# Optimization experiments

Hardware: AMD Instinct MI355X
Metric: run time of the kernel (lower is better)

The kernel has to match this reference:

```python
import jax, jax.numpy as jnp
import numpy as np

N = 200000
NNZ = 6400000
E = 500000
IN_P, IN_F, IN_N = 62, 37, 37
HID, LAT, DEC_HID = 256, 128, 64


def _p(key, shape, scale=0.05):
    return scale * jax.random.normal(key, shape, dtype=jnp.float32)


def setup_inputs() -> dict:
    key = jax.random.key(0)
    ks = jax.random.split(key, 32)
    inp = {
        'x_process': jax.random.normal(ks[0], (N, IN_P), dtype=jnp.float32),
        'x_file': jax.random.normal(ks[1], (N, IN_F), dtype=jnp.float32),
        'x_network': jax.random.normal(ks[2], (N, IN_N), dtype=jnp.float32),
        'adj_rows': jax.random.randint(ks[3], (NNZ,), 0, N, dtype=jnp.int32),
        'adj_cols': jax.random.randint(ks[4], (NNZ,), 0, N, dtype=jnp.int32),
        'adj_vals': jax.random.uniform(ks[5], (NNZ,), dtype=jnp.float32) / 32.0,
        'edge_src': jax.random.randint(ks[6], (E,), 0, N, dtype=jnp.int32),
        'edge_dst': jax.random.randint(ks[7], (E,), 0, N, dtype=jnp.int32),
        # per-view encoder params (weights stored [in, out])
        'Wp1': _p(ks[8], (IN_P, HID)), 'bp1': jnp.zeros((HID,), jnp.float32),
        'Wp2': _p(ks[9], (HID, LAT)), 'bp2': jnp.zeros((LAT,), jnp.float32),
        'Wf1': _p(ks[10], (IN_F, HID)), 'bf1': jnp.zeros((HID,), jnp.float32),
        'Wf2': _p(ks[11], (HID, LAT)), 'bf2': jnp.zeros((LAT,), jnp.float32),
        'Wn1': _p(ks[12], (IN_N, HID)), 'bn1': jnp.zeros((HID,), jnp.float32),
        'Wn2': _p(ks[13], (HID, LAT)), 'bn2': jnp.zeros((LAT,), jnp.float32),
        # gates
        'Wgp': _p(ks[14], (LAT, 1)), 'bgp': jnp.zeros((1,), jnp.float32),
        'Wgf': _p(ks[15], (LAT, 1)), 'bgf': jnp.zeros((1,), jnp.float32),
        'Wgn': _p(ks[16], (LAT, 1)), 'bgn': jnp.zeros((1,), jnp.float32),
        # mlp edge decoder
        'Wd1': _p(ks[17], (4 * LAT, DEC_HID)), 'bd1': jnp.zeros((DEC_HID,), jnp.float32),
        'Wd2': _p(ks[18], (DEC_HID, 1)), 'bd2': jnp.zeros((1,), jnp.float32),
    }
    return inp


def _spmm(rows, cols, vals, x):
    # sparse (COO) adjacency @ dense x : gather cols, scale, scatter-add into rows
    return jax.ops.segment_sum(vals[:, None] * x[cols], rows, num_segments=N)


def _encode_view(x, rows, cols, vals, W1, b1, W2, b2):
    h = jax.nn.relu(_spmm(rows, cols, vals, x) @ W1 + b1)  # dropout=0 / eval mode
    return _spmm(rows, cols, vals, h) @ W2 + b2


def reference(x_process, x_file, x_network, adj_rows, adj_cols, adj_vals,
              edge_src, edge_dst,
              Wp1, bp1, Wp2, bp2, Wf1, bf1, Wf2, bf2, Wn1, bn1, Wn2, bn2,
              Wgp, bgp, Wgf, bgf, Wgn, bgn, Wd1, bd1, Wd2, bd2):
    zp = _encode_view(x_process, adj_rows, adj_cols, adj_vals, Wp1, bp1, Wp2, bp2)
    zf = _encode_view(x_file, adj_rows, adj_cols, adj_vals, Wf1, bf1, Wf2, bf2)
    zn = _encode_view(x_network, adj_rows, adj_cols, adj_vals, Wn1, bn1, Wn2, bn2)
    # multi-view softmax gating -> fused latent [N, LAT]
    scores = jnp.concatenate([zp @ Wgp + bgp, zf @ Wgf + bgf, zn @ Wgn + bgn], axis=1)
    alpha = jax.nn.softmax(scores, axis=1)
    z = alpha[:, 0:1] * zp + alpha[:, 1:2] * zf + alpha[:, 2:3] * zn
    # mlp edge decoder: gather src/dst, concat features, small MLP
    zs, zd = z[edge_src], z[edge_dst]
    feats = jnp.concatenate([zs, zd, zs * zd, jnp.abs(zs - zd)], axis=1)  # [E, 4*LAT]
    logits = jax.nn.relu(feats @ Wd1 + bd1) @ Wd2 + bd2
    return logits[:, 0]
```

## Files before the change

### kernel.cpp

```cpp
#include <hip/hip_runtime.h>
#include <math.h>

#define Nn 200000
#define NNZV 6400000
#define NE 500000
#define HID 256
#define LAT 128

typedef _Float16 h2 __attribute__((ext_vector_type(2)));
typedef _Float16 f16x8 __attribute__((ext_vector_type(8)));
typedef float f32x4 __attribute__((ext_vector_type(4)));
typedef short s16x8 __attribute__((ext_vector_type(8)));
struct alignas(8) H4 { _Float16 h[4]; };

__device__ __forceinline__ float rdlanef(float v, int k){
  return __uint_as_float(__builtin_amdgcn_readlane(__float_as_uint(v), k));
}

__global__ __launch_bounds__(256) void k_zero(int* __restrict__ cnt){
  int i = blockIdx.x*256 + threadIdx.x;
  if(i < Nn) cnt[i] = 0;
}

__global__ __launch_bounds__(256) void k_count(const int* __restrict__ rows, int* __restrict__ cnt){
  int i = blockIdx.x*256 + threadIdx.x;
  if(i < NNZV) atomicAdd(&cnt[rows[i]], 1);
}

__global__ __launch_bounds__(512) void k_scan_block(const int* __restrict__ cnt, int* __restrict__ incl, int* __restrict__ bsum){
  __shared__ int s[512];
  int t = threadIdx.x;
  int i = blockIdx.x*512 + t;
  int v = (i < Nn) ? cnt[i] : 0;
  s[t] = v; __syncthreads();
  for(int off = 1; off < 512; off <<= 1){
    int x = (t >= off) ? s[t-off] : 0;
    __syncthreads();
    s[t] += x;
    __syncthreads();
  }
  if(i < Nn) incl[i] = s[t];
  if(t == 511) bsum[blockIdx.x] = s[t];
}

__global__ __launch_bounds__(512) void k_scan_bsum(int* __restrict__ bsum, int nb){
  __shared__ int s[512];
  int t = threadIdx.x;
  int v = (t < nb) ? bsum[t] : 0;
  s[t] = v; __syncthreads();
  for(int off = 1; off < 512; off <<= 1){
    int x = (t >= off) ? s[t-off] : 0;
    __syncthreads();
    s[t] += x;
    __syncthreads();
  }
  if(t < nb) bsum[t] = s[t] - v;
}

__global__ __launch_bounds__(256) void k_finish(const int* __restrict__ incl, const int* __restrict__ boff, int* __restrict__ row_ptr){
  int i = blockIdx.x*256 + threadIdx.x;
  if(i < Nn) row_ptr[i+1] = incl[i] + boff[i >> 9];
  if(i == 0) row_ptr[0] = 0;
}

__global__ __launch_bounds__(256) void k_initcur(const int* __restrict__ row_ptr, int* __restrict__ cur){
  int i = blockIdx.x*256 + threadIdx.x;
  if(i < Nn) cur[i] = row_ptr[i];
}

__global__ __launch_bounds__(256) void k_scatter(const int* __restrict__ rows, const int* __restrict__ cols,
    const float* __restrict__ vals, int* __restrict__ cur,
    int* __restrict__ cols_s, _Float16* __restrict__ vals_s){
  int i = blockIdx.x*256 + threadIdx.x;
  if(i >= NNZV) return;
  int r = rows[i];
  int j = atomicAdd(&cur[r], 1);
  cols_s[j] = cols[i];
  vals_s[j] = (_Float16)vals[i];
}

__global__ __launch_bounds__(256) void k_xpack(const float* __restrict__ xp, const float* __restrict__ xf,
    const float* __restrict__ xn, _Float16* __restrict__ xc0, _Float16* __restrict__ xtl){
  int idx = blockIdx.x*256 + threadIdx.x;
  int row = idx/18, c8 = idx - row*18;
  if(row >= Nn) return;
  H4 ha, hb;
  #pragma unroll
  for(int q = 0; q < 8; q++){
    int c = c8*8 + q;
    float x;
    if(c < 62)       x = xp[row*62 + c];
    else if(c < 99)  x = xf[row*37 + (c-62)];
    else if(c == 99) x = 0.f;
    else if(c < 137) x = xn[row*37 + (c-100)];
    else             x = 0.f;
    if(q < 4) ha.h[q] = (_Float16)x; else hb.h[q-4] = (_Float16)x;
  }
  if(c8 < 16){
    *(H4*)&xc0[(size_t)row*128 + c8*8]     = ha;
    *(H4*)&xc0[(size_t)row*128 + c8*8 + 4] = hb;
  } else {
    int t = (c8-16)*8;
    *(H4*)&xtl[(size_t)row*16 + t]     = ha;
    *(H4*)&xtl[(size_t)row*16 + t + 4] = hb;
  }
}

__global__ __launch_bounds__(256) void k_wpackF(
    const float* __restrict__ Wp1, const float* __restrict__ Wf1, const float* __restrict__ Wn1,
    const float* __restrict__ Wp2, const float* __restrict__ Wf2, const float* __restrict__ Wn2,
    _Float16* __restrict__ w1fp, _Float16* __restrict__ w1ff, _Float16* __restrict__ w1fn,
    _Float16* __restrict__ w2fp, _Float16* __restrict__ w2ff, _Float16* __restrict__ w2fn){
  int i = blockIdx.x*256 + threadIdx.x;
  if(i >= 18432) return;
  int v = i / 6144, rem = i - v*6144;
  const float* W1 = (v==0)?Wp1:((v==1)?Wf1:Wn1);
  const float* W2 = (v==0)?Wp2:((v==1)?Wf2:Wn2);
  _Float16* d1 = (v==0)?w1fp:((v==1)?w1ff:w1fn);
  _Float16* d2 = (v==0)?w2fp:((v==1)?w2ff:w2fn);
  int Kv = (v==0)?62:37;
  f16x8 o;
  if(rem < 2048){
    int kt = rem >> 10, r2 = rem & 1023;
    int nt = r2 >> 6, l = r2 & 63;
    int krow = kt*32 + (l>>4)*8, col = nt*16 + (l&15);
    #pragma unroll
    for(int j = 0; j < 8; j++){
      int k = krow + j;
      o[j] = (k < Kv) ? (_Float16)W1[k*256 + col] : (_Float16)0.f;
    }
    *(f16x8*)&d1[rem*8] = o;
  } else {
    int r = rem - 2048;
    int kt = r >> 9, nt = (r >> 6) & 7, l = r & 63;
    int krow = kt*32 + (l>>4)*8, col = nt*16 + (l&15);
    #pragma unroll
    for(int j = 0; j < 8; j++)
      o[j] = (_Float16)W2[(krow + j)*128 + col];
    *(f16x8*)&d2[r*8] = o;
  }
}

__global__ void k_wg2(const float* __restrict__ Wp2, const float* __restrict__ Wgp,
                      const float* __restrict__ Wf2, const float* __restrict__ Wgf,
                      const float* __restrict__ Wn2, const float* __restrict__ Wgn,
                      float* __restrict__ wg2){
  int k = threadIdx.x;
  float p = 0.f, f = 0.f, n = 0.f;
  for(int c = 0; c < 128; c++){
    p = fmaf(Wp2[k*128 + c], Wgp[c], p);
    f = fmaf(Wf2[k*128 + c], Wgf[c], f);
    n = fmaf(Wn2[k*128 + c], Wgn[c], n);
  }
  wg2[k] = p; wg2[256 + k] = f; wg2[512 + k] = n;
}

__global__ void k_const(const float* b2p, const float* Wgp, const float* bgp,
                        const float* b2f, const float* Wgf, const float* bgf,
                        const float* b2n, const float* Wgn, const float* bgn,
                        float* c3){
  int l = threadIdx.x;
  float p = 0.f, f = 0.f, n = 0.f;
  for(int j = l; j < LAT; j += 64){
    p += b2p[j]*Wgp[j];
    f += b2f[j]*Wgf[j];
    n += b2n[j]*Wgn[j];
  }
  #pragma unroll
  for(int off = 32; off >= 1; off >>= 1){
    p += __shfl_xor(p, off);
    f += __shfl_xor(f, off);
    n += __shfl_xor(n, off);
  }
  if(l == 0){ c3[0] = p + bgp[0]; c3[1] = f + bgf[0]; c3[2] = n + bgn[0]; }
}

__device__ __forceinline__ void encode_view(
    int tid, int row0, int voff, int Kv, int vidx,
    const _Float16 (*sT)[152], _Float16 (*sTv)[72], _Float16 (*hT)[264],
    const _Float16* __restrict__ w1frag, const float* __restrict__ b1,
    const _Float16* __restrict__ w2frag, const float* __restrict__ wg2v,
    _Float16* __restrict__ Y3, float* __restrict__ yg4f){
  int w = tid >> 6, l = tid & 63;
  int kg = l >> 4, er = l & 15;
  int mrow = (w & 1)*16 + er;

  {
    int row = tid >> 3, c0 = (tid & 7)*8;
    f16x8 vv;
    #pragma unroll
    for(int q = 0; q < 8; q++){
      int c = c0 + q;
      vv[q] = (c < Kv) ? sT[row][voff + c] : (_Float16)0.f;
    }
    *(f16x8*)&sTv[row][c0] = vv;
  }
  __syncthreads();

  {
    f16x8 a0 = *(const f16x8*)&sTv[mrow][kg*8];
    f16x8 a1 = *(const f16x8*)&sTv[mrow][32 + kg*8];
    int ntb = (w >> 1)*8;
    #pragma unroll
    for(int nt8 = 0; nt8 < 8; nt8++){
      int nt = ntb + nt8;
      f16x8 b0 = *(const f16x8*)&w1frag[(size_t)((0*16 + nt)*64 + l)*8];
      f16x8 b1v = *(const f16x8*)&w1frag[(size_t)((1*16 + nt)*64 + l)*8];
      f32x4 acc = {0.f, 0.f, 0.f, 0.f};
      acc = __builtin_amdgcn_mfma_f32_16x16x32_f16(a0, b0, acc, 0, 0, 0);
      acc = __builtin_amdgcn_mfma_f32_16x16x32_f16(a1, b1v, acc, 0, 0, 0);
      int col = nt*16 + er;
      float bb = b1[col];
      #pragma unroll
      for(int j = 0; j < 4; j++)
        hT[(w & 1)*16 + kg*4 + j][col] = (_Float16)fmaxf(acc[j] + bb, 0.f);
    }
  }
  __syncthreads();

  {
    int row = tid >> 3, cg = tid & 7;
    float p = 0.f;
    #pragma unroll 8
    for(int kk = 0; kk < 32; kk++)
      p = fmaf((float)hT[row][cg*32 + kk], wg2v[cg*32 + kk], p);
    p += __shfl_xor(p, 1);
    p += __shfl_xor(p, 2);
    p += __shfl_xor(p, 4);
    if((tid & 7) == 0) yg4f[(size_t)(row0 + row)*4 + vidx] = p;
  }

  {
    f16x8 af[8];
    #pragma unroll
    for(int kt = 0; kt < 8; kt++)
      af[kt] = *(const f16x8*)&hT[mrow][kt*32 + kg*8];
    int ntb = (w >> 1)*4;
    #pragma unroll
    for(int nt4 = 0; nt4 < 4; nt4++){
      int nt = ntb + nt4;
      f32x4 acc = {0.f, 0.f, 0.f, 0.f};
      #pragma unroll
      for(int kt = 0; kt < 8; kt++){
        f16x8 bf = *(const f16x8*)&w2frag[(size_t)((kt*8 + nt)*64 + l)*8];
        acc = __builtin_amdgcn_mfma_f32_16x16x32_f16(af[kt], bf, acc, 0, 0, 0);
      }
      int col = nt*16 + er;
      #pragma unroll
      for(int j = 0; j < 4; j++)
        Y3[(size_t)(row0 + (w & 1)*16 + kg*4 + j)*384 + vidx*128 + col] = (_Float16)acc[j];
    }
  }
  __syncthreads();
}

__global__ __launch_bounds__(256, 5) void k_encfused(
    const int* __restrict__ row_ptr, const int* __restrict__ cols_s, const _Float16* __restrict__ vals_s,
    const _Float16* __restrict__ xc0, const _Float16* __restrict__ xtl,
    const _Float16* __restrict__ w1fp, const float* __restrict__ bp1, const _Float16* __restrict__ w2fp,
    const _Float16* __restrict__ w1ff, const float* __restrict__ bf1, const _Float16* __restrict__ w2ff,
    const _Float16* __restrict__ w1fn, const float* __restrict__ bn1, const _Float16* __restrict__ w2fn,
    const float* __restrict__ wg2,
    _Float16* __restrict__ Y3, float* __restrict__ yg4f){
  __shared__ _Float16 sT[32][152];
  __shared__ _Float16 sTv[32][72];
  __shared__ _Float16 hT[32][264];
  int tid = threadIdx.x;
  int lane = tid & 63, wid = tid >> 6;
  int row0 = blockIdx.x * 32;
  bool hast = (lane < 8);

  for(int rr8 = 0; rr8 < 8; rr8++){
    int r = row0 + wid*8 + rr8;
    int start = row_ptr[r], end = row_ptr[r+1];
    float a0 = 0.f, a1 = 0.f, a2 = 0.f, a3 = 0.f;
    for(int j0 = start; j0 < end; j0 += 64){
      int m = end - j0; if(m > 64) m = 64;
      int mycol = 0; float myval = 0.f;
      if(lane < m){ mycol = cols_s[j0 + lane]; myval = (float)vals_s[j0 + lane]; }
      int mpad = (m + 3) & ~3;
      for(int k = 0; k < mpad; k += 4){
        #pragma unroll
        for(int q = 0; q < 4; q++){
          int c = __builtin_amdgcn_readlane(mycol, k + q);
          float v = rdlanef(myval, k + q);
          h2 xa = *(const h2*)((const char*)xc0 + (((unsigned)c) << 8) + lane*4);
          a0 = fmaf((float)xa[0], v, a0);
          a1 = fmaf((float)xa[1], v, a1);
          if(hast){
            h2 xb = *(const h2*)((const char*)xtl + ((unsigned)c)*32 + lane*4);
            a2 = fmaf((float)xb[0], v, a2);
            a3 = fmaf((float)xb[1], v, a3);
          }
        }
      }
    }
    int rr = wid*8 + rr8;
    h2 s01; s01[0] = (_Float16)a0; s01[1] = (_Float16)a1;
    *(h2*)&sT[rr][2*lane] = s01;
    if(hast){
      h2 s23; s23[0] = (_Float16)a2; s23[1] = (_Float16)a3;
      *(h2*)&sT[rr][128 + 2*lane] = s23;
    }
  }
  __syncthreads();

  encode_view(tid, row0, 0,   62, 0, sT, sTv, hT, w1fp, bp1, w2fp, wg2,       Y3, yg4f);
  encode_view(tid, row0, 62,  37, 1, sT, sTv, hT, w1ff, bf1, w2ff, wg2 + 256, Y3, yg4f);
  encode_view(tid, row0, 100, 37, 2, sT, sTv, hT, w1fn, bn1, w2fn, wg2 + 512, Y3, yg4f);
}

__global__ __launch_bounds__(256, 8) void k_spmm2f(
    const int* __restrict__ row_ptr, const int* __restrict__ cols_s, const _Float16* __restrict__ vals_s,
    const _Float16* __restrict__ Y3,
    const float4* __restrict__ yg4, const float* __restrict__ c3,
    const float* __restrict__ b2p, const float* __restrict__ b2f, const float* __restrict__ b2n,
    _Float16* __restrict__ z){
  int tid = threadIdx.x;
  int lane = tid & 63;
  int r = blockIdx.x*4 + (tid >> 6);
  int start = row_ptr[r], end = row_ptr[r+1];
  unsigned lo = lane*4;
  float ap0=0.f, ap1=0.f, af0=0.f, af1=0.f, an0=0.f, an1=0.f;
  float scp=0.f, scf=0.f, scn=0.f;
  const char* Yb = (const char*)Y3;
  for(int j0 = start; j0 < end; j0 += 64){
    int m = end - j0; if(m > 64) m = 64;
    int mycol = 0; float myval = 0.f;
    if(lane < m){
      mycol = cols_s[j0 + lane];
      myval = (float)vals_s[j0 + lane];
      float4 g = yg4[mycol];
      scp = fmaf(myval, g.x, scp);
      scf = fmaf(myval, g.y, scf);
      scn = fmaf(myval, g.z, scn);
    }
    int mpad = (m + 3) & ~3;
    for(int k = 0; k < mpad; k += 4){
      #pragma unroll
      for(int q = 0; q < 4; q++){
        int c = __builtin_amdgcn_readlane(mycol, k + q);
        float v = rdlanef(myval, k + q);
        const char* p = Yb + ((unsigned)c)*768u + lo;
        h2 yp = *(const h2*)(p);
        h2 yf = *(const h2*)(p + 256);
        h2 yn = *(const h2*)(p + 512);
        ap0 = fmaf((float)yp[0], v, ap0); ap1 = fmaf((float)yp[1], v, ap1);
        af0 = fmaf((float)yf[0], v, af0); af1 = fmaf((float)yf[1], v, af1);
        an0 = fmaf((float)yn[0], v, an0); an1 = fmaf((float)yn[1], v, an1);
      }
    }
  }
  #pragma unroll
  for(int off = 32; off >= 1; off >>= 1){
    scp += __shfl_xor(scp, off);
    scf += __shfl_xor(scf, off);
    scn += __shfl_xor(scn, off);
  }
  float sp = scp + c3[0], sf = scf + c3[1], sn = scn + c3[2];
  float mx = fmaxf(sp, fmaxf(sf, sn));
  float ep = expf(sp - mx), ef = expf(sf - mx), en = expf(sn - mx);
  float inv = 1.f / (ep + ef + en);
  float A0 = ep*inv, A1 = ef*inv, A2 = en*inv;
  int o = lane*2;
  float2 bp = *(const float2*)&b2p[o];
  float2 bf = *(const float2*)&b2f[o];
  float2 bn = *(const float2*)&b2n[o];
  float z0 = A0*(ap0 + bp.x) + A1*(af0 + bf.x) + A2*(an0 + bn.x);
  float z1 = A0*(ap1 + bp.y) + A1*(af1 + bf.y) + A2*(an1 + bn.y);
  h2 uz; uz[0] = (_Float16)z0; uz[1] = (_Float16)z1;
  *(h2*)&z[(size_t)r*LAT + o] = uz;
}

#define DEC_TILES (NE/16)
__global__ __launch_bounds__(256) void k_dec(
    const _Float16* __restrict__ z, const int* __restrict__ esrc, const int* __restrict__ edst,
    const float* __restrict__ Wd1, const float* __restrict__ bd1,
    const float* __restrict__ Wd2, const float* __restrict__ bd2, float* __restrict__ out){
  __shared__ float part[4][16][68];
  int tid = threadIdx.x;
  int w  = tid >> 6;
  int l  = tid & 63;
  int erow = l & 15;
  int kg   = l >> 4;

  f16x8 bfr[4][4];
  #pragma unroll
  for(int kt = 0; kt < 4; kt++){
    #pragma unroll
    for(int nt = 0; nt < 4; nt++){
      f16x8 bb;
      #pragma unroll
      for(int j = 0; j < 8; j++)
        bb[j] = (_Float16)Wd1[(w*128 + kt*32 + kg*8 + j)*64 + nt*16 + erow];
      bfr[kt][nt] = bb;
    }
  }

  int n0 = (tid & 15) * 4;
  int e2 = tid >> 4;
  float4 bb1 = *(const float4*)&bd1[n0];
  float4 w2v = *(const float4*)&Wd2[n0];
  float bias2 = bd2[0];

  for(int tile = blockIdx.x; tile < DEC_TILES; tile += gridDim.x){
    int e = tile*16 + erow;
    int si = esrc[e], di = edst[e];
    const f16x8* zs = (const f16x8*)&z[(size_t)si*LAT];
    const f16x8* zd = (const f16x8*)&z[(size_t)di*LAT];
    f16x8 afr[4];
    if(w == 0){
      #pragma unroll
      for(int kt = 0; kt < 4; kt++) afr[kt] = zs[kt*4 + kg];
    } else if(w == 1){
      #pragma unroll
      for(int kt = 0; kt < 4; kt++) afr[kt] = zd[kt*4 + kg];
    } else if(w == 2){
      #pragma unroll
      for(int kt = 0; kt < 4; kt++) afr[kt] = zs[kt*4 + kg] * zd[kt*4 + kg];
    } else {
      #pragma unroll
      for(int kt = 0; kt < 4; kt++){
        f16x8 d = zs[kt*4 + kg] - zd[kt*4 + kg];
        s16x8 m = __builtin_bit_cast(s16x8, d) & (short)0x7fff;
        afr[kt] = __builtin_bit_cast(f16x8, m);
      }
    }
    f32x4 zero = {0.f, 0.f, 0.f, 0.f};
    f32x4 acc[4] = {zero, zero, zero, zero};
    #pragma unroll
    for(int kt = 0; kt < 4; kt++){
      #pragma unroll
      for(int nt = 0; nt < 4; nt++)
        acc[nt] = __builtin_amdgcn_mfma_f32_16x16x32_f16(afr[kt], bfr[kt][nt], acc[nt], 0, 0, 0);
    }
    #pragma unroll
    for(int nt = 0; nt < 4; nt++){
      #pragma unroll
      for(int j = 0; j < 4; j++)
        part[w][kg*4 + j][nt*16 + erow] = acc[nt][j];
    }
    __syncthreads();
    float s0 = part[0][e2][n0+0] + part[1][e2][n0+0] + part[2][e2][n0+0] + part[3][e2][n0+0];
    float s1 = part[0][e2][n0+1] + part[1][e2][n0+1] + part[2][e2][n0+1] + part[3][e2][n0+1];
    float s2 = part[0][e2][n0+2] + part[1][e2][n0+2] + part[2][e2][n0+2] + part[3][e2][n0+2];
    float s3 = part[0][e2][n0+3] + part[1][e2][n0+3] + part[2][e2][n0+3] + part[3][e2][n0+3];
    float p = fmaxf(s0 + bb1.x, 0.f)*w2v.x + fmaxf(s1 + bb1.y, 0.f)*w2v.y
            + fmaxf(s2 + bb1.z, 0.f)*w2v.z + fmaxf(s3 + bb1.w, 0.f)*w2v.w;
    #pragma unroll
    for(int off = 1; off < 16; off <<= 1) p += __shfl_xor(p, off);
    if((tid & 15) == 0) out[tile*16 + e2] = p + bias2;
    __syncthreads();
  }
}

extern "C" void kernel_launch(void* const* d_in, const int* in_sizes, int n_in,
                              void* d_out, int out_size, void* d_ws, size_t ws_size,
                              hipStream_t stream) {
  const float* xp  = (const float*)d_in[0];
  const float* xf  = (const float*)d_in[1];
  const float* xn  = (const float*)d_in[2];
  const int* arows = (const int*)d_in[3];
  const int* acols = (const int*)d_in[4];
  const float* avals = (const float*)d_in[5];
  const int* esrc  = (const int*)d_in[6];
  const int* edst  = (const int*)d_in[7];
  const float* Wp1 = (const float*)d_in[8];  const float* bp1 = (const float*)d_in[9];
  const float* Wp2 = (const float*)d_in[10]; const float* bp2 = (const float*)d_in[11];
  const float* Wf1 = (const float*)d_in[12]; const float* bf1 = (const float*)d_in[13];
  const float* Wf2 = (const float*)d_in[14]; const float* bf2w = (const float*)d_in[15];
  const float* Wn1 = (const float*)d_in[16]; const float* bn1 = (const float*)d_in[17];
  const float* Wn2 = (const float*)d_in[18]; const float* bn2 = (const float*)d_in[19];
  const float* Wgp = (const float*)d_in[20]; const float* bgp = (const float*)d_in[21];
  const float* Wgf = (const float*)d_in[22]; const float* bgf = (const float*)d_in[23];
  const float* Wgn = (const float*)d_in[24]; const float* bgn = (const float*)d_in[25];
  const float* Wd1 = (const float*)d_in[26]; const float* bd1 = (const float*)d_in[27];
  const float* Wd2 = (const float*)d_in[28]; const float* bd2 = (const float*)d_in[29];
  float* out = (float*)d_out;
  (void)in_sizes; (void)n_in; (void)out_size; (void)ws_size;

  char* base = (char*)d_ws;
  size_t off = 0;
  auto alloc = [&](size_t nbytes) -> char* {
    off = (off + 255) & ~(size_t)255;
    char* p = base + off;
    off += nbytes;
    return p;
  };
  int*      row_ptr = (int*)     alloc((size_t)(Nn + 1) * 4);
  int*      cols_s  = (int*)     alloc((size_t)NNZV * 4);
  _Float16* vals_s  = (_Float16*)alloc((size_t)NNZV * 2);
  _Float16* xcat0   = (_Float16*)alloc((size_t)Nn * 128 * 2);
  _Float16* xtail   = (_Float16*)alloc((size_t)Nn * 16 * 2);
  _Float16* Y3      = (_Float16*)alloc((size_t)Nn * 384 * 2);
  float*    yg4     = (float*)   alloc((size_t)Nn * 4 * 4);
  float*    c3      = (float*)   alloc(256);
  float*    wg2     = (float*)   alloc(3 * 256 * 4);
  _Float16* w1fp = (_Float16*)alloc(16384*2);
  _Float16* w1ff = (_Float16*)alloc(16384*2);
  _Float16* w1fn = (_Float16*)alloc(16384*2);
  _Float16* w2fp = (_Float16*)alloc(32768*2);
  _Float16* w2ff = (_Float16*)alloc(32768*2);
  _Float16* w2fn = (_Float16*)alloc(32768*2);
  _Float16* z = xcat0;
  int* cur  = (int*)((char*)xcat0);
  int* incl = (int*)((char*)xcat0 + 1000000);
  int* bsum = (int*)((char*)xcat0 + 2000000);

  int NB = (Nn + 511) / 512;

  k_zero   <<<(Nn + 255)/256, 256, 0, stream>>>(cur);
  k_count  <<<(NNZV + 255)/256, 256, 0, stream>>>(arows, cur);
  k_scan_block<<<NB, 512, 0, stream>>>(cur, incl, bsum);
  k_scan_bsum<<<1, 512, 0, stream>>>(bsum, NB);
  k_finish <<<(Nn + 255)/256, 256, 0, stream>>>(incl, bsum, row_ptr);
  k_initcur<<<(Nn + 255)/256, 256, 0, stream>>>(row_ptr, cur);
  k_scatter<<<(NNZV + 255)/256, 256, 0, stream>>>(arows, acols, avals, cur, cols_s, vals_s);

  k_xpack<<<(Nn*18 + 255)/256, 256, 0, stream>>>(xp, xf, xn, xcat0, xtail);
  k_wpackF<<<72, 256, 0, stream>>>(Wp1, Wf1, Wn1, Wp2, Wf2, Wn2,
                                   w1fp, w1ff, w1fn, w2fp, w2ff, w2fn);
  k_wg2<<<1, 256, 0, stream>>>(Wp2, Wgp, Wf2, Wgf, Wn2, Wgn, wg2);
  k_const<<<1, 64, 0, stream>>>(bp2, Wgp, bgp, bf2w, Wgf, bgf, bn2, Wgn, bgn, c3);

  k_encfused<<<Nn/32, 256, 0, stream>>>(row_ptr, cols_s, vals_s, xcat0, xtail,
      w1fp, bp1, w2fp,  w1ff, bf1, w2ff,  w1fn, bn1, w2fn,  wg2,
      Y3, yg4);

  k_spmm2f<<<Nn/4, 256, 0, stream>>>(row_ptr, cols_s, vals_s, Y3,
      (const float4*)yg4, c3, bp2, bf2w, bn2, z);

  k_dec<<<2048, 256, 0, stream>>>(z, esrc, edst, Wd1, bd1, Wd2, bd2, out);
}
```

Baseline: 2.535 ms.

## Process two rows per wavefront in first SpMM and stage Y3 stores via LDS

The first-layer aggregation in the fused encoder now splits each wavefront into two 32-lane halves, each handling its own row. Each lane loads 8-byte f16x4 gathers instead of 4-byte pairs, and column/value broadcasts use shuffles instead of readlane. This doubles the bytes per gather instruction and halves the row-loop trip count, at the cost of divergence when the two rows differ in length. Separately, the MFMA output tile is written into shared memory (reusing hT) and then stored to Y3 as contiguous 16-byte vectors instead of scattered 2-byte stores, which adds two barriers.

```diff
diff --git a/kernel.cpp b/kernel.cpp
--- a/kernel.cpp
+++ b/kernel.cpp
@@ -8,6 +8,7 @@
 #define LAT 128
 
 typedef _Float16 h2 __attribute__((ext_vector_type(2)));
+typedef _Float16 f16x4 __attribute__((ext_vector_type(4)));
 typedef _Float16 f16x8 __attribute__((ext_vector_type(8)));
 typedef float f32x4 __attribute__((ext_vector_type(4)));
 typedef short s16x8 __attribute__((ext_vector_type(8)));
@@ -235,6 +236,8 @@
     #pragma unroll
     for(int kt = 0; kt < 8; kt++)
       af[kt] = *(const f16x8*)&hT[mrow][kt*32 + kg*8];
+    __syncthreads();
+    _Float16* yst = &hT[0][0];
     int ntb = (w >> 1)*4;
     #pragma unroll
     for(int nt4 = 0; nt4 < 4; nt4++){
@@ -248,8 +251,15 @@
       int col = nt*16 + er;
       #pragma unroll
       for(int j = 0; j < 4; j++)
-        Y3[(size_t)(row0 + (w & 1)*16 + kg*4 + j)*384 + vidx*128 + col] = (_Float16)acc[j];
-    }
+        yst[((w & 1)*16 + kg*4 + j)*132 + col] = (_Float16)acc[j];
+    }
+    __syncthreads();
+    int row = tid >> 3, c0 = (tid & 7)*16;
+    f16x8 y0 = *(const f16x8*)&yst[row*132 + c0];
+    f16x8 y1 = *(const f16x8*)&yst[row*132 + c0 + 8];
+    _Float16* yo = &Y3[(size_t)(row0 + row)*384 + vidx*128 + c0];
+    *(f16x8*)yo       = y0;
+    *(f16x8*)(yo + 8) = y1;
   }
   __syncthreads();
 }
@@ -267,40 +277,62 @@
   __shared__ _Float16 hT[32][264];
   int tid = threadIdx.x;
   int lane = tid & 63, wid = tid >> 6;
+  int hl = lane & 31;
+  int half = lane >> 5;
+  int base = lane & 32;
   int row0 = blockIdx.x * 32;
-  bool hast = (lane < 8);
-
-  for(int rr8 = 0; rr8 < 8; rr8++){
-    int r = row0 + wid*8 + rr8;
+  bool hast = (hl < 4);
+  const char* xc0b = (const char*)xc0;
+  const char* xtlb = (const char*)xtl;
+
+  for(int p = 0; p < 4; p++){
+    int rr = wid*8 + p*2 + half;
+    int r = row0 + rr;
     int start = row_ptr[r], end = row_ptr[r+1];
+    int len = end - start;
+    int lenO = __shfl(len, lane ^ 32);
+    int lenmax = len > lenO ? len : lenO;
     float a0 = 0.f, a1 = 0.f, a2 = 0.f, a3 = 0.f;
-    for(int j0 = start; j0 < end; j0 += 64){
-      int m = end - j0; if(m > 64) m = 64;
+    float t0 = 0.f, t1 = 0.f, t2 = 0.f, t3 = 0.f;
+    for(int j0 = 0; j0 < lenmax; j0 += 32){
+      int m = len - j0; if(m > 32) m = 32; if(m < 0) m = 0;
+      int mO = lenO - j0; if(mO > 32) mO = 32; if(mO < 0) mO = 0;
+      int mmax = m > mO ? m : mO;
       int mycol = 0; float myval = 0.f;
-      if(lane < m){ mycol = cols_s[j0 + lane]; myval = (float)vals_s[j0 + lane]; }
-      int mpad = (m + 3) & ~3;
+      if(hl < m){
+        mycol = cols_s[start + j0 + hl];
+        myval = (float)vals_s[start + j0 + hl];
+      }
+      int mpad = (mmax + 3) & ~3;
       for(int k = 0; k < mpad; k += 4){
         #pragma unroll
         for(int q = 0; q < 4; q++){
-          int c = __builtin_amdgcn_readlane(mycol, k + q);
-          float v = rdlanef(myval, k + q);
-          h2 xa = *(const h2*)((const char*)xc0 + (((unsigned)c) << 8) + lane*4);
+          int c = __shfl(mycol, base + k + q);
+          float v = __shfl(myval, base + k + q);
+          f16x4 xa = *(const f16x4*)(xc0b + (((unsigned)c) << 8) + hl*8);
           a0 = fmaf((float)xa[0], v, a0);
           a1 = fmaf((float)xa[1], v, a1);
+          a2 = fmaf((float)xa[2], v, a2);
+          a3 = fmaf((float)xa[3], v, a3);
           if(hast){
-            h2 xb = *(const h2*)((const char*)xtl + ((unsigned)c)*32 + lane*4);
-            a2 = fmaf((float)xb[0], v, a2);
-            a3 = fmaf((float)xb[1], v, a3);
+            f16x4 xb = *(const f16x4*)(xtlb + ((unsigned)c)*32u + hl*8);
+            t0 = fmaf((float)xb[0], v, t0);
+            t1 = fmaf((float)xb[1], v, t1);
+            t2 = fmaf((float)xb[2], v, t2);
+            t3 = fmaf((float)xb[3], v, t3);
           }
         }
       }
     }
-    int rr = wid*8 + rr8;
     h2 s01; s01[0] = (_Float16)a0; s01[1] = (_Float16)a1;
-    *(h2*)&sT[rr][2*lane] = s01;
+    h2 s23; s23[0] = (_Float16)a2; s23[1] = (_Float16)a3;
+    *(h2*)&sT[rr][4*hl]     = s01;
+    *(h2*)&sT[rr][4*hl + 2] = s23;
     if(hast){
-      h2 s23; s23[0] = (_Float16)a2; s23[1] = (_Float16)a3;
-      *(h2*)&sT[rr][128 + 2*lane] = s23;
+      h2 u01; u01[0] = (_Float16)t0; u01[1] = (_Float16)t1;
+      h2 u23; u23[0] = (_Float16)t2; u23[1] = (_Float16)t3;
+      *(h2*)&sT[rr][128 + 4*hl]     = u01;
+      *(h2*)&sT[rr][128 + 4*hl + 2] = u23;
     }
   }
   __syncthreads();
```

Measured after the change: 2.292 ms. 1.11x faster.
